# Kernel optimization log

Measured on AMD Instinct MI355X. Metric: run time of the kernel, lower is better.

## Reference

```python
import jax, jax.numpy as jnp
import numpy as np

N_HEAD, D_K, D_V, D_MODEL = 8, 64, 64, 512
LN_EPS = 1e-5

def setup_inputs() -> dict:
    key = jax.random.key(0)
    k1, k2, k3 = jax.random.split(key, 3)
    B, C, H, W = 8, D_MODEL, 32, 32
    q = jax.random.normal(k1, (B, C, H, W), dtype=jnp.float32)
    w_qkvs = jax.random.normal(k2, (N_HEAD * D_K, D_MODEL), dtype=jnp.float32) * np.sqrt(2.0 / (D_MODEL + D_K))
    fc_w = jax.random.normal(k3, (D_MODEL, N_HEAD * D_V), dtype=jnp.float32) * np.sqrt(2.0 / (N_HEAD * D_V + D_MODEL))
    fc_b = jnp.zeros((D_MODEL,), dtype=jnp.float32)
    ln_gamma = jnp.ones((D_MODEL,), dtype=jnp.float32)
    ln_beta = jnp.zeros((D_MODEL,), dtype=jnp.float32)
    return {"q": q, "w_qkvs": w_qkvs, "fc_w": fc_w, "fc_b": fc_b,
            "ln_gamma": ln_gamma, "ln_beta": ln_beta}

def reference(q, w_qkvs, fc_w, fc_b, ln_gamma, ln_beta):
    B, C, H, W = q.shape
    L = H * W
    temp = np.sqrt(D_K).astype(np.float32)
    # [B, C, H, W] -> [B, L, C] tokens
    x = q.reshape(B, C, L).transpose(0, 2, 1)
    residual = x
    # shared QKV projection -> per-head [B, h, L, d]
    qh = (x @ w_qkvs.T).reshape(B, L, N_HEAD, D_K).transpose(0, 2, 1, 3)
    # self-attention: q = k = v = qh
    scores = jnp.einsum('bhqd,bhkd->bhqk', qh, qh) / temp
    attn = jax.nn.softmax(scores, axis=-1)  # dropout is identity in eval
    out = jnp.einsum('bhqk,bhkd->bhqd', attn, qh)  # [B, h, L, d_v]
    # merge heads: [B, L, h*d_v]
    out = out.transpose(0, 2, 1, 3).reshape(B, L, N_HEAD * D_V)
    out = out @ fc_w.T + fc_b
    y = out + residual
    mu = jnp.mean(y, axis=-1, keepdims=True)
    var = jnp.mean(jnp.square(y - mu), axis=-1, keepdims=True)
    y = (y - mu) / jnp.sqrt(var + LN_EPS) * ln_gamma + ln_beta
    # raw reshape, matching torch .view(B, -1, H, W)
    return y.reshape(B, -1, H, W)
```

## Files before the change

### kernel.cpp

```cpp
#include <hip/hip_runtime.h>
#include <stdint.h>

#define BATCH 8
#define LTOK 1024
#define DMODEL 512
#define NHEAD 8
#define DHEAD 64

typedef unsigned short u16;
typedef u16 u16x8 __attribute__((ext_vector_type(8)));
typedef short bf16x8 __attribute__((ext_vector_type(8)));
typedef float f32x4 __attribute__((ext_vector_type(4)));

#define MFMA16(a,b,c) __builtin_amdgcn_mfma_f32_16x16x32_bf16((a),(b),(c),0,0,0)

__device__ __forceinline__ float bf2f(u16 x){
  union{unsigned u; float f;} v; v.u = ((unsigned)x)<<16; return v.f;
}
__device__ __forceinline__ u16 f2bf(float f){
  union{float f; unsigned u;} v; v.f = f;
  unsigned r = v.u + 0x7fffu + ((v.u>>16)&1u);
  return (u16)(r>>16);
}

__device__ __forceinline__ void gload_lds16(const u16* g, u16* l){
  __builtin_amdgcn_global_load_lds(
      (const __attribute__((address_space(1))) void*)g,
      (__attribute__((address_space(3))) void*)l,
      16, 0, 0);
}

__global__ __launch_bounds__(256) void convert_k(const float* __restrict__ src,
                                                 u16* __restrict__ dst, int n){
  const int i = (blockIdx.x*256 + threadIdx.x)*8;
  if (i >= n) return;
  u16x8 v;
  #pragma unroll
  for (int j=0;j<8;j++) v[j] = f2bf(src[i+j]);
  *(u16x8*)(dst + i) = v;
}

__global__ __launch_bounds__(256) void transpose_f2b(const float* __restrict__ src,
                                                     u16* __restrict__ dst,
                                                     int R, int C){
  __shared__ __align__(16) u16 t[64][72];
  const int b  = blockIdx.z;
  const int r0 = blockIdx.x*64, c0 = blockIdx.y*64;
  const float* s = src + (size_t)b*R*C;
  u16* d         = dst + (size_t)b*R*C;
  const int tid = threadIdx.x;
  const int row = tid>>3, ch = (tid&7)*8;
  #pragma unroll
  for (int rr=0; rr<64; rr+=32){
    const float* p = s + (size_t)(r0+row+rr)*C + c0 + ch;
    u16x8 v;
    #pragma unroll
    for (int j=0;j<8;j++) v[j] = f2bf(p[j]);
    *(u16x8*)&t[row+rr][ch] = v;
  }
  __syncthreads();
  #pragma unroll
  for (int rr=0; rr<64; rr+=32){
    const int dr = row+rr;
    u16x8 v;
    #pragma unroll
    for (int j=0;j<8;j++) v[j] = t[ch+j][dr];
    *(u16x8*)(d + (size_t)(c0+dr)*R + r0 + ch) = v;
  }
}

__device__ __forceinline__ void stage_gemm(const u16* __restrict__ src,
                                           int row0, int k0, u16* lds, int tid){
  #pragma unroll
  for (int s2=0; s2<2; ++s2){
    const int slot = tid + s2*256;
    const int row = slot>>3, ch8 = slot&7;
    const int k = k0 + ((ch8 ^ (row&7))<<3);
    gload_lds16(src + (size_t)(row0+row)*DMODEL + k, lds + slot*8);
  }
}

__global__ __launch_bounds__(256) void qkv_gemm(const u16* __restrict__ A,
                                                const u16* __restrict__ W,
                                                u16* __restrict__ qh,
                                                u16* __restrict__ vt){
  __shared__ __align__(128) u16 sA[2][4096];
  __shared__ __align__(128) u16 sB[2][4096];
  const int m0 = blockIdx.x*64, n0 = blockIdx.y*64;
  const int tid = threadIdx.x, w = tid>>6, lane = tid&63;
  const int wr = w>>1, wc = w&1;
  const int lr = lane&15, lg = lane>>4;
  f32x4 acc[2][2] = {};
  stage_gemm(A, m0, 0, sA[0], tid);
  stage_gemm(W, n0, 0, sB[0], tid);
  int buf = 0;
  for (int kt=0; kt<8; ++kt){
    __syncthreads();
    if (kt < 7){
      stage_gemm(A, m0, (kt+1)*64, sA[buf^1], tid);
      stage_gemm(W, n0, (kt+1)*64, sB[buf^1], tid);
    }
    #pragma unroll
    for (int ks=0; ks<2; ++ks){
      bf16x8 af[2], bfr[2];
      #pragma unroll
      for (int mi=0; mi<2; ++mi){
        const int r = wr*32 + mi*16 + lr;
        af[mi] = *(const bf16x8*)(&sA[buf][(r*64 + ks*32 + lg*8) ^ ((r&7)<<3)]);
      }
      #pragma unroll
      for (int nj=0; nj<2; ++nj){
        const int r = wc*32 + nj*16 + lr;
        bfr[nj] = *(const bf16x8*)(&sB[buf][(r*64 + ks*32 + lg*8) ^ ((r&7)<<3)]);
      }
      #pragma unroll
      for (int mi=0; mi<2; ++mi)
        #pragma unroll
        for (int nj=0; nj<2; ++nj)
          acc[mi][nj] = MFMA16(af[mi], bfr[nj], acc[mi][nj]);
    }
    buf ^= 1;
  }
  #pragma unroll
  for (int mi=0; mi<2; ++mi)
    #pragma unroll
    for (int nj=0; nj<2; ++nj)
      #pragma unroll
      for (int r=0; r<4; ++r){
        const int m = m0 + wr*32 + mi*16 + lg*4 + r;
        const int n = n0 + wc*32 + nj*16 + lr;
        const int bb = m>>10, l = m&1023, hh = n>>6, d = n&63;
        const int bh = bb*NHEAD + hh;
        const int t = l>>6, rr = l&63;
        const u16 val = f2bf(acc[mi][nj][r]);
        qh[(size_t)(bh*16 + t)*4096 + ((rr*64 + d) ^ ((rr&7)<<3))] = val;
        vt[(size_t)(bh*16 + t)*4096 + ((d*64 + rr) ^ ((d&7)<<3))]  = val;
      }
}

__global__ __launch_bounds__(512) void attn_k(const u16* __restrict__ qh,
                                              const u16* __restrict__ vt,
                                              u16* __restrict__ ao){
  __shared__ __align__(128) u16 sK[2][4096];
  __shared__ __align__(128) u16 sV[2][4096];
  __shared__ __align__(128) u16 sP[8192];
  const int bid = blockIdx.x;
  const int qt = bid >> 6, bh = bid & 63;
  const int b = bh >> 3, h = bh & 7;
  const u16* Kb = qh + (size_t)bh*16*4096;
  const u16* Vb = vt + (size_t)bh*16*4096;
  const int tid = threadIdx.x, w = tid>>6, lane = tid&63;
  const int lr = lane&15, lg = lane>>4;
  const int wp = w*1024;

  bf16x8 aq[2];
  {
    const u16* Qt = Kb + (size_t)(qt*2 + (w>>2))*4096;
    const int rq = (w&3)*16 + lr;
    #pragma unroll
    for (int ks=0; ks<2; ++ks){
      u16x8 v = *(const u16x8*)(Qt + ((rq*64 + ks*32 + lg*8) ^ ((rq&7)<<3)));
      bf16x8 t;
      #pragma unroll
      for (int j=0;j<8;j++) t[j] = (short)f2bf(bf2f(v[j])*0.18033688f);
      aq[ks] = t;
    }
  }

  f32x4 o[4] = {};
  float lsum[4] = {0.f,0.f,0.f,0.f};

  gload_lds16(Kb + tid*8, sK[0] + tid*8);
  gload_lds16(Vb + tid*8, sV[0] + tid*8);
  __syncthreads();

  int buf = 0;
  for (int kt=0; kt<16; ++kt){
    if (kt+1 < 16){
      gload_lds16(Kb + (size_t)(kt+1)*4096 + tid*8, sK[buf^1] + tid*8);
      gload_lds16(Vb + (size_t)(kt+1)*4096 + tid*8, sV[buf^1] + tid*8);
    }
    f32x4 sc[4] = {};
    #pragma unroll
    for (int ks=0; ks<2; ++ks){
      #pragma unroll
      for (int nj=0; nj<4; ++nj){
        const int rk = nj*16 + lr;
        bf16x8 bk = *(const bf16x8*)(&sK[buf][(rk*64 + ks*32 + lg*8) ^ ((rk&7)<<3)]);
        sc[nj] = MFMA16(aq[ks], bk, sc[nj]);
      }
    }
    #pragma unroll
    for (int nj=0; nj<4; ++nj){
      #pragma unroll
      for (int r=0; r<4; ++r){
        const float p = __builtin_amdgcn_exp2f(sc[nj][r]);
        const unsigned pu = __float_as_uint(p) & 0xFFFF0000u;
        lsum[r] += __uint_as_float(pu);
        const int prow = lg*4 + r;
        sP[wp + ((prow*64 + nj*16 + lr) ^ ((prow&7)<<3))] = (u16)(pu>>16);
      }
    }
    asm volatile("s_waitcnt lgkmcnt(0)" ::: "memory");
    #pragma unroll
    for (int ks=0; ks<2; ++ks){
      bf16x8 pa = *(const bf16x8*)(&sP[wp + ((lr*64 + ks*32 + lg*8) ^ ((lr&7)<<3))]);
      #pragma unroll
      for (int dj=0; dj<4; ++dj){
        const int rB = dj*16 + lr;
        bf16x8 bv = *(const bf16x8*)(&sV[buf][(rB*64 + ks*32 + lg*8) ^ ((rB&7)<<3)]);
        o[dj] = MFMA16(pa, bv, o[dj]);
      }
    }
    __syncthreads();
    buf ^= 1;
  }

  float inv[4];
  #pragma unroll
  for (int r=0; r<4; ++r){
    float s = lsum[r];
    s += __shfl_xor(s,1); s += __shfl_xor(s,2);
    s += __shfl_xor(s,4); s += __shfl_xor(s,8);
    inv[r] = __builtin_amdgcn_rcpf(s);
  }
  const int i0 = qt*128 + w*16;
  #pragma unroll
  for (int dj=0; dj<4; ++dj)
    #pragma unroll
    for (int r=0; r<4; ++r){
      const int l = i0 + lg*4 + r;
      const int d = dj*16 + lr;
      ao[((size_t)(b*LTOK + l))*DMODEL + h*DHEAD + d] = f2bf(o[dj][r]*inv[r]);
    }
}

__global__ __launch_bounds__(256) void fc_gemm(const u16* __restrict__ A,
                                               const u16* __restrict__ W,
                                               const float* __restrict__ bias,
                                               const u16* __restrict__ resid,
                                               u16* __restrict__ Y){
  __shared__ __align__(128) u16 sA[2][4096];
  __shared__ __align__(128) u16 sB[2][4096];
  const int m0 = blockIdx.x*64, n0 = blockIdx.y*64;
  const int tid = threadIdx.x, w = tid>>6, lane = tid&63;
  const int wr = w>>1, wc = w&1;
  const int lr = lane&15, lg = lane>>4;
  f32x4 acc[2][2] = {};
  stage_gemm(A, m0, 0, sA[0], tid);
  stage_gemm(W, n0, 0, sB[0], tid);
  int buf = 0;
  for (int kt=0; kt<8; ++kt){
    __syncthreads();
    if (kt < 7){
      stage_gemm(A, m0, (kt+1)*64, sA[buf^1], tid);
      stage_gemm(W, n0, (kt+1)*64, sB[buf^1], tid);
    }
    #pragma unroll
    for (int ks=0; ks<2; ++ks){
      bf16x8 af[2], bfr[2];
      #pragma unroll
      for (int mi=0; mi<2; ++mi){
        const int r = wr*32 + mi*16 + lr;
        af[mi] = *(const bf16x8*)(&sA[buf][(r*64 + ks*32 + lg*8) ^ ((r&7)<<3)]);
      }
      #pragma unroll
      for (int nj=0; nj<2; ++nj){
        const int r = wc*32 + nj*16 + lr;
        bfr[nj] = *(const bf16x8*)(&sB[buf][(r*64 + ks*32 + lg*8) ^ ((r&7)<<3)]);
      }
      #pragma unroll
      for (int mi=0; mi<2; ++mi)
        #pragma unroll
        for (int nj=0; nj<2; ++nj)
          acc[mi][nj] = MFMA16(af[mi], bfr[nj], acc[mi][nj]);
    }
    buf ^= 1;
  }
  #pragma unroll
  for (int mi=0; mi<2; ++mi)
    #pragma unroll
    for (int nj=0; nj<2; ++nj)
      #pragma unroll
      for (int r=0; r<4; ++r){
        const int m = m0 + wr*32 + mi*16 + lg*4 + r;
        const int n = n0 + wc*32 + nj*16 + lr;
        const float val = acc[mi][nj][r] + bias[n] + bf2f(resid[(size_t)m*DMODEL+n]);
        Y[(size_t)m*DMODEL+n] = f2bf(val);
      }
}

__global__ __launch_bounds__(256) void ln_k(const u16* __restrict__ Y,
                                            const float* __restrict__ gamma,
                                            const float* __restrict__ beta,
                                            float* __restrict__ out){
  const int row = blockIdx.x*4 + (threadIdx.x>>6);
  const int lane = threadIdx.x&63;
  const u16* yr = Y + (size_t)row*DMODEL;
  u16x8 v = *(const u16x8*)(yr + lane*8);
  float x[8]; float s=0.f, sq=0.f;
  #pragma unroll
  for (int j=0;j<8;j++){ x[j]=bf2f(v[j]); s+=x[j]; sq+=x[j]*x[j]; }
  #pragma unroll
  for (int mk=1; mk<64; mk<<=1){ s += __shfl_xor(s,mk); sq += __shfl_xor(sq,mk); }
  const float mean = s*(1.f/DMODEL);
  float var = sq*(1.f/DMODEL) - mean*mean;
  const float rstd = rsqrtf(var + 1e-5f);
  float* po = out + (size_t)row*DMODEL + lane*8;
  #pragma unroll
  for (int j=0;j<8;j++){
    const int c = lane*8+j;
    po[j] = (x[j]-mean)*rstd*gamma[c] + beta[c];
  }
}

extern "C" void kernel_launch(void* const* d_in, const int* in_sizes, int n_in,
                              void* d_out, int out_size, void* d_ws, size_t ws_size,
                              hipStream_t stream){
  (void)in_sizes; (void)n_in; (void)out_size; (void)ws_size;
  const float* q      = (const float*)d_in[0];
  const float* w_qkvs = (const float*)d_in[1];
  const float* fc_w   = (const float*)d_in[2];
  const float* fc_b   = (const float*)d_in[3];
  const float* ln_g   = (const float*)d_in[4];
  const float* ln_b   = (const float*)d_in[5];
  float* out = (float*)d_out;
  char* ws = (char*)d_ws;
  u16* x_rm  = (u16*)(ws);
  u16* qh_sw = (u16*)(ws + 8388608);
  u16* vtt   = (u16*)(ws + 16777216);
  u16* ao    = (u16*)(ws + 25165824);
  u16* wqkvb = (u16*)(ws + 33554432);
  u16* wfcb  = (u16*)(ws + 34078720);
  u16* y0    = qh_sw;

  convert_k<<<128,256,0,stream>>>(w_qkvs, wqkvb, DMODEL*DMODEL);
  convert_k<<<128,256,0,stream>>>(fc_w,   wfcb,  DMODEL*DMODEL);
  transpose_f2b<<<dim3(8,16,BATCH),256,0,stream>>>(q, x_rm, DMODEL, LTOK);
  qkv_gemm<<<dim3(128,8),256,0,stream>>>(x_rm, wqkvb, qh_sw, vtt);
  attn_k<<<512,512,0,stream>>>(qh_sw, vtt, ao);
  fc_gemm<<<dim3(128,8),256,0,stream>>>(ao, wfcb, fc_b, x_rm, y0);
  ln_k<<<2048,256,0,stream>>>(y0, ln_g, ln_b, out);
}
```

Before: 81.68 us.

## Read K/V fragments directly from global memory in attention, drop LDS staging

The attention kernel stops staging K and V tiles in double-buffered shared memory and instead loads MFMA fragments straight from global memory (via L2/L1), with the QKV GEMM writing plain row-major Q/K and transposed V layouts without swizzle. Blocks shrink to 256 threads covering 64 query rows, so the grid doubles to 1024 blocks, and s_setprio hints are placed around the MFMA phases. This removes the per-tile __syncthreads and LDS traffic and may raise occupancy, but each wave now issues uncoalesced 16-byte global loads with no explicit prefetching, so memory latency is exposed.

```diff
diff --git a/kernel.cpp b/kernel.cpp
--- a/kernel.cpp
+++ b/kernel.cpp
@@ -131,35 +131,31 @@
         const int n = n0 + wc*32 + nj*16 + lr;
         const int bb = m>>10, l = m&1023, hh = n>>6, d = n&63;
         const int bh = bb*NHEAD + hh;
-        const int t = l>>6, rr = l&63;
         const u16 val = f2bf(acc[mi][nj][r]);
-        qh[(size_t)(bh*16 + t)*4096 + ((rr*64 + d) ^ ((rr&7)<<3))] = val;
-        vt[(size_t)(bh*16 + t)*4096 + ((d*64 + rr) ^ ((d&7)<<3))]  = val;
-      }
-}
-
-__global__ __launch_bounds__(512) void attn_k(const u16* __restrict__ qh,
+        qh[(size_t)bh*LTOK*DHEAD + (size_t)l*DHEAD + d] = val;
+        vt[(size_t)bh*DHEAD*LTOK + (size_t)d*LTOK + l] = val;
+      }
+}
+
+__global__ __launch_bounds__(256) void attn_k(const u16* __restrict__ qh,
                                               const u16* __restrict__ vt,
                                               u16* __restrict__ ao){
-  __shared__ __align__(128) u16 sK[2][4096];
-  __shared__ __align__(128) u16 sV[2][4096];
-  __shared__ __align__(128) u16 sP[8192];
+  __shared__ __align__(128) u16 sP[4096];
   const int bid = blockIdx.x;
   const int qt = bid >> 6, bh = bid & 63;
   const int b = bh >> 3, h = bh & 7;
-  const u16* Kb = qh + (size_t)bh*16*4096;
-  const u16* Vb = vt + (size_t)bh*16*4096;
+  const u16* Kb = qh + (size_t)bh*LTOK*DHEAD;
+  const u16* Vb = vt + (size_t)bh*DHEAD*LTOK;
   const int tid = threadIdx.x, w = tid>>6, lane = tid&63;
   const int lr = lane&15, lg = lane>>4;
   const int wp = w*1024;
 
   bf16x8 aq[2];
   {
-    const u16* Qt = Kb + (size_t)(qt*2 + (w>>2))*4096;
-    const int rq = (w&3)*16 + lr;
-    #pragma unroll
-    for (int ks=0; ks<2; ++ks){
-      u16x8 v = *(const u16x8*)(Qt + ((rq*64 + ks*32 + lg*8) ^ ((rq&7)<<3)));
+    const int rq = qt*64 + w*16 + lr;
+    #pragma unroll
+    for (int ks=0; ks<2; ++ks){
+      u16x8 v = *(const u16x8*)(Kb + (size_t)rq*DHEAD + ks*32 + lg*8);
       bf16x8 t;
       #pragma unroll
       for (int j=0;j<8;j++) t[j] = (short)f2bf(bf2f(v[j])*0.18033688f);
@@ -170,26 +166,19 @@
   f32x4 o[4] = {};
   float lsum[4] = {0.f,0.f,0.f,0.f};
 
-  gload_lds16(Kb + tid*8, sK[0] + tid*8);
-  gload_lds16(Vb + tid*8, sV[0] + tid*8);
-  __syncthreads();
-
-  int buf = 0;
   for (int kt=0; kt<16; ++kt){
-    if (kt+1 < 16){
-      gload_lds16(Kb + (size_t)(kt+1)*4096 + tid*8, sK[buf^1] + tid*8);
-      gload_lds16(Vb + (size_t)(kt+1)*4096 + tid*8, sV[buf^1] + tid*8);
-    }
     f32x4 sc[4] = {};
+    __builtin_amdgcn_s_setprio(1);
     #pragma unroll
     for (int ks=0; ks<2; ++ks){
       #pragma unroll
       for (int nj=0; nj<4; ++nj){
-        const int rk = nj*16 + lr;
-        bf16x8 bk = *(const bf16x8*)(&sK[buf][(rk*64 + ks*32 + lg*8) ^ ((rk&7)<<3)]);
+        const int rk = kt*64 + nj*16 + lr;
+        bf16x8 bk = *(const bf16x8*)(Kb + (size_t)rk*DHEAD + ks*32 + lg*8);
         sc[nj] = MFMA16(aq[ks], bk, sc[nj]);
       }
     }
+    __builtin_amdgcn_s_setprio(0);
     #pragma unroll
     for (int nj=0; nj<4; ++nj){
       #pragma unroll
@@ -202,18 +191,18 @@
       }
     }
     asm volatile("s_waitcnt lgkmcnt(0)" ::: "memory");
+    __builtin_amdgcn_s_setprio(1);
     #pragma unroll
     for (int ks=0; ks<2; ++ks){
       bf16x8 pa = *(const bf16x8*)(&sP[wp + ((lr*64 + ks*32 + lg*8) ^ ((lr&7)<<3))]);
       #pragma unroll
       for (int dj=0; dj<4; ++dj){
-        const int rB = dj*16 + lr;
-        bf16x8 bv = *(const bf16x8*)(&sV[buf][(rB*64 + ks*32 + lg*8) ^ ((rB&7)<<3)]);
+        const int d = dj*16 + lr;
+        bf16x8 bv = *(const bf16x8*)(Vb + (size_t)d*LTOK + kt*64 + ks*32 + lg*8);
         o[dj] = MFMA16(pa, bv, o[dj]);
       }
     }
-    __syncthreads();
-    buf ^= 1;
+    __builtin_amdgcn_s_setprio(0);
   }
 
   float inv[4];
@@ -224,7 +213,7 @@
     s += __shfl_xor(s,4); s += __shfl_xor(s,8);
     inv[r] = __builtin_amdgcn_rcpf(s);
   }
-  const int i0 = qt*128 + w*16;
+  const int i0 = qt*64 + w*16;
   #pragma unroll
   for (int dj=0; dj<4; ++dj)
     #pragma unroll
@@ -338,7 +327,7 @@
   convert_k<<<128,256,0,stream>>>(fc_w,   wfcb,  DMODEL*DMODEL);
   transpose_f2b<<<dim3(8,16,BATCH),256,0,stream>>>(q, x_rm, DMODEL, LTOK);
   qkv_gemm<<<dim3(128,8),256,0,stream>>>(x_rm, wqkvb, qh_sw, vtt);
-  attn_k<<<512,512,0,stream>>>(qh_sw, vtt, ao);
+  attn_k<<<1024,256,0,stream>>>(qh_sw, vtt, ao);
   fc_gemm<<<dim3(128,8),256,0,stream>>>(ao, wfcb, fc_b, x_rm, y0);
   ln_k<<<2048,256,0,stream>>>(y0, ln_g, ln_b, out);
 }
```

Result: slower. 163.2 us (+99.9%).
